# Optimization experiments

Hardware: AMD Instinct MI355X
Metric: run time of the kernel (lower is better)

## Reference

```python
import jax, jax.numpy as jnp
import numpy as np

S_DIM = 512
H2 = 512          # 2 * h_dim, listener feature dim
ATTN = 128
NUM_CLASS = 64
B, T, N = 64, 512, 128
IN_DIM = NUM_CLASS + H2  # LSTM layer-0 input dim


def _p(key, shape, scale=0.05):
    return scale * jax.random.normal(key, shape, dtype=jnp.float32)


def setup_inputs() -> dict:
    key = jax.random.key(0)
    ks = jax.random.split(key, 20)
    inp = {
        "x": jax.random.randint(ks[0], (B, N), 0, NUM_CLASS),
        "h": jax.random.normal(ks[1], (B, T, H2), dtype=jnp.float32),
        # LSTM layer 0 (PyTorch gate order i,f,g,o stacked along dim 0)
        "Wih0": _p(ks[2], (4 * S_DIM, IN_DIM)),
        "Whh0": _p(ks[3], (4 * S_DIM, S_DIM)),
        "bih0": _p(ks[4], (4 * S_DIM,)),
        "bhh0": _p(ks[5], (4 * S_DIM,)),
        # LSTM layer 1
        "Wih1": _p(ks[6], (4 * S_DIM, S_DIM)),
        "Whh1": _p(ks[7], (4 * S_DIM, S_DIM)),
        "bih1": _p(ks[8], (4 * S_DIM,)),
        "bhh1": _p(ks[9], (4 * S_DIM,)),
        # attention projections phi (on s) and psi (on h)
        "Wphi": _p(ks[10], (ATTN, S_DIM)),
        "bphi": _p(ks[11], (ATTN,)),
        "Wpsi": _p(ks[12], (ATTN, H2)),
        "bpsi": _p(ks[13], (ATTN,)),
        # character distribution
        "Wcd": _p(ks[14], (NUM_CLASS, S_DIM + H2)),
        "bcd": _p(ks[15], (NUM_CLASS,)),
    }
    return inp


def _lstm_cell(x, hs, cs, Wih, Whh, bih, bhh):
    g = x @ Wih.T + bih + hs @ Whh.T + bhh
    i, f, gg, o = jnp.split(g, 4, axis=-1)
    c_new = jax.nn.sigmoid(f) * cs + jax.nn.sigmoid(i) * jnp.tanh(gg)
    h_new = jax.nn.sigmoid(o) * jnp.tanh(c_new)
    return h_new, c_new


def reference(x, h, Wih0, Whh0, bih0, bhh0, Wih1, Whh1, bih1, bhh1,
              Wphi, bphi, Wpsi, bpsi, Wcd, bcd):
    # Teacher forcing (tf_rate=1.0): next rnn input char is ground truth x[:, t].
    bs = h.shape[0]
    onehots = jax.nn.one_hot(x, NUM_CLASS, dtype=h.dtype)          # [B, N, C]
    onehots = jnp.transpose(onehots, (1, 0, 2))                    # [N, B, C]
    psi_h = h @ Wpsi.T + bpsi                                      # [B, T, ATTN]

    zeros = jnp.zeros((bs, S_DIM), dtype=h.dtype)
    init = (zeros, zeros, zeros, zeros, h[:, 0, :])                # h1,c1,h2,c2,ctx

    def step(carry, onehot_t):
        h1, c1, h2, c2, ctx = carry
        inp = jnp.concatenate([onehot_t, ctx], axis=-1)            # [B, C+H2]
        h1, c1 = _lstm_cell(inp, h1, c1, Wih0, Whh0, bih0, bhh0)
        h2, c2 = _lstm_cell(h1, h2, c2, Wih1, Whh1, bih1, bhh1)
        s = h2                                                     # [B, S_DIM]
        phi_s = s @ Wphi.T + bphi                                  # [B, ATTN]
        e = jnp.einsum('bd,btd->bt', phi_s, psi_h)                 # [B, T]
        alpha = jax.nn.softmax(e, axis=-1)
        c_ctx = jnp.einsum('bt,btd->bd', alpha, h)                 # [B, H2]
        p = jnp.concatenate([s, c_ctx], axis=-1) @ Wcd.T + bcd     # [B, C]
        return (h1, c1, h2, c2, c_ctx), p

    _, ps = jax.lax.scan(step, init, onehots)                      # [N, B, C]
    return jnp.transpose(ps, (1, 0, 2))                            # [B, N, C]
```

## Files before the change

kernel.cpp:

```cpp
#include <hip/hip_runtime.h>
#include <hip/hip_bf16.h>
#include <math.h>

#define BB 64
#define TT 512
#define NS 128
#define SD 512
#define ATT 128
#define NC 64
#define KX 1024

typedef __attribute__((ext_vector_type(8))) short bf8;
typedef __attribute__((ext_vector_type(4))) float f4;

__device__ __forceinline__ float sigm(float x) { return 1.0f / (1.0f + expf(-x)); }
__device__ __forceinline__ float b2f(short s) {
    union { unsigned u; float f; } c; c.u = ((unsigned)(unsigned short)s) << 16; return c.f;
}
#define MFMA16(a, b, c) __builtin_amdgcn_mfma_f32_16x16x32_bf16((a), (b), (c), 0, 0, 0)

__device__ __forceinline__ void st_sc(__hip_bfloat16* p, float val) {
    __hip_bfloat16 hb(val);
    unsigned short bits; __builtin_memcpy(&bits, &hb, 2);
    unsigned v = bits;
    asm volatile("global_store_short %0, %1, off sc0 sc1" :: "v"(p), "v"(v) : "memory");
}
__device__ __forceinline__ void st_u32_sc(unsigned* p, unsigned v) {
    asm volatile("global_store_dword %0, %1, off sc0 sc1" :: "v"(p), "v"(v) : "memory");
}
__device__ __forceinline__ unsigned ld_u32_sc(const unsigned* p) {
    unsigned v;
    asm volatile("global_load_dword %0, %1, off sc0 sc1\ns_waitcnt vmcnt(0)"
                 : "=v"(v) : "v"(p) : "memory");
    return v;
}

__device__ __forceinline__ void gsync(unsigned* arrv, unsigned* rel, unsigned tk)
{
    __syncthreads();
    if (blockIdx.x == 0) {
        if (threadIdx.x > 0 && threadIdx.x < 256) {
            while (ld_u32_sc(arrv + threadIdx.x * 32) < tk)
                __builtin_amdgcn_s_sleep(2);
        }
        __syncthreads();
        if (threadIdx.x < 8)
            st_u32_sc(rel + threadIdx.x * 32, tk);
    } else {
        if (threadIdx.x == 0) {
            st_u32_sc(arrv + blockIdx.x * 32, tk);
            while (ld_u32_sc(rel + (blockIdx.x & 7) * 32) < tk)
                __builtin_amdgcn_s_sleep(2);
        }
        __syncthreads();
    }
}

template<int BASE>
__device__ __forceinline__ f4 gemm16r(const __hip_bfloat16* Xrow, int quad,
                                      const bf8 (&wreg)[32], f4 acc)
{
    const bf8* Bq = (const bf8*)Xrow + quad;
    bf8 r[16];
#pragma unroll
    for (int i = 0; i < 16; ++i) r[i] = Bq[(BASE + i) * 4];
#pragma unroll
    for (int i = 0; i < 16; ++i) acc = MFMA16(wreg[BASE + i], r[i], acc);
    return acc;
}

__global__ void f2b_kernel(const float* __restrict__ src, __hip_bfloat16* __restrict__ dst, int n)
{
    int i = (blockIdx.x * blockDim.x + threadIdx.x) * 4;
    if (i < n) {
        float4 v = *(const float4*)(src + i);
        dst[i]     = __hip_bfloat16(v.x);
        dst[i + 1] = __hip_bfloat16(v.y);
        dst[i + 2] = __hip_bfloat16(v.z);
        dst[i + 3] = __hip_bfloat16(v.w);
    }
}

__global__ __launch_bounds__(256) void transpose_h_kernel(const float* __restrict__ h,
                                                          __hip_bfloat16* __restrict__ hT)
{
    int bidx = blockIdx.x;
    int b = bidx >> 6, tt0 = ((bidx >> 3) & 7) * 64, dd0 = (bidx & 7) * 64;
    __shared__ __hip_bfloat16 tile[64][65];
    int dd = threadIdx.x & 63, r4 = threadIdx.x >> 6;
#pragma unroll
    for (int i = 0; i < 64; i += 4) {
        int tl = i + r4;
        tile[tl][dd] = __hip_bfloat16(h[((size_t)b * TT + tt0 + tl) * SD + dd0 + dd]);
    }
    __syncthreads();
#pragma unroll
    for (int i = 0; i < 64; i += 4) {
        int dl = i + r4;
        hT[((size_t)b * SD + dd0 + dl) * TT + tt0 + dd] = tile[dd][dl];
    }
}

__global__ void prep_w1_kernel(const float* __restrict__ Wih, const float* __restrict__ Whh,
                               __hip_bfloat16* __restrict__ W)
{
    int idx = blockIdx.x * blockDim.x + threadIdx.x;
    if (idx >= 2048 * KX) return;
    int np = idx >> 10, kk = idx & 1023;
    int q = np & 3, d = np >> 2, j = q * 512 + d;
    float v = (kk < 512) ? Wih[j * 576 + 64 + kk] : Whh[j * 512 + kk - 512];
    W[idx] = __hip_bfloat16(v);
}

__global__ void prep_w2_kernel(const float* __restrict__ Wih, const float* __restrict__ Whh,
                               __hip_bfloat16* __restrict__ W)
{
    int idx = blockIdx.x * blockDim.x + threadIdx.x;
    if (idx >= 2048 * KX) return;
    int np = idx >> 10, kk = idx & 1023;
    int q = np & 3, d = np >> 2, j = q * 512 + d;
    float v = (kk < 512) ? Wih[j * 512 + kk] : Whh[j * 512 + kk - 512];
    W[idx] = __hip_bfloat16(v);
}

__global__ void prep_misc_kernel(const float* __restrict__ Wih0,
                                 const float* __restrict__ bih0, const float* __restrict__ bhh0,
                                 const float* __restrict__ bih1, const float* __restrict__ bhh1,
                                 float* __restrict__ b1v, float* __restrict__ b2v,
                                 float* __restrict__ woh)
{
    int idx = blockIdx.x * blockDim.x + threadIdx.x;
    if (idx >= 64 * 512) return;
    int tok = idx >> 9, d = idx & 511;
    float4 w;
    w.x = Wih0[(0 * 512 + d) * 576 + tok];
    w.y = Wih0[(1 * 512 + d) * 576 + tok];
    w.z = Wih0[(2 * 512 + d) * 576 + tok];
    w.w = Wih0[(3 * 512 + d) * 576 + tok];
    ((float4*)woh)[idx] = w;
    if (tok == 0) {
        float4 b1, b2;
        b1.x = bih0[d] + bhh0[d];             b1.y = bih0[512 + d] + bhh0[512 + d];
        b1.z = bih0[1024 + d] + bhh0[1024 + d]; b1.w = bih0[1536 + d] + bhh0[1536 + d];
        b2.x = bih1[d] + bhh1[d];             b2.y = bih1[512 + d] + bhh1[512 + d];
        b2.z = bih1[1024 + d] + bhh1[1024 + d]; b2.w = bih1[1536 + d] + bhh1[1536 + d];
        ((float4*)b1v)[d] = b1;
        ((float4*)b2v)[d] = b2;
    }
}

__global__ void init_kernel(const float* __restrict__ h,
                            __hip_bfloat16* __restrict__ X1_0,
                            __hip_bfloat16* __restrict__ X2_0,
                            float* __restrict__ c1, float* __restrict__ c2,
                            unsigned* __restrict__ bar)
{
    int idx = blockIdx.x * blockDim.x + threadIdx.x;
    if (idx >= 64 * KX) return;
    int b = idx >> 10, col = idx & 1023;
    __hip_bfloat16 z(0.0f);
    X1_0[idx] = (col < 512) ? __hip_bfloat16(h[(size_t)b * TT * SD + col]) : z;
    X2_0[idx] = z;
    if (idx < 512 * 64) { c1[idx] = 0.f; c2[idx] = 0.f; }
    if (idx < 16384) bar[idx] = 0u;
}

__global__ __launch_bounds__(512, 1) void decode_kernel(
    const __hip_bfloat16* __restrict__ W1, const __hip_bfloat16* __restrict__ W2,
    const __hip_bfloat16* __restrict__ Wphib, const float* __restrict__ bphi,
    const __hip_bfloat16* __restrict__ psib, const __hip_bfloat16* __restrict__ hT,
    __hip_bfloat16* X1base, __hip_bfloat16* X2base,
    __hip_bfloat16* scb, const int* __restrict__ xtok,
    const float* __restrict__ b1v, const float* __restrict__ b2v,
    const float* __restrict__ woh, unsigned* __restrict__ bar)
{
    __shared__ bf8 hTl[128 * 64];
    __shared__ float h2s[512], phis[128], es[512], red[512], wred[16];

    const int bid = blockIdx.x, tid = threadIdx.x;
    const int lane = tid & 63, w = tid >> 6;
    const int mr = lane & 15, quad = lane >> 4;
    const bool isA = bid < 128;
    const int ab = (bid & 7) * 8 + ((bid >> 3) & 7), dch = bid >> 6;

    unsigned* arrv = bar;
    unsigned* rel  = bar + 256 * 32;

    bf8 wreg[32];
    if (tid < 256) {
        const __hip_bfloat16* Wg = isA ? W1 : W2;
        const int m0 = (bid & 127) * 16;
        const bf8* src = (const bf8*)(Wg + (size_t)(m0 + mr) * KX) + quad;
#pragma unroll
        for (int ko = 0; ko < 32; ++ko) wreg[ko] = src[ko * 4];
    }
    {
        const bf8* src = (const bf8*)hT + ((size_t)ab * SD + dch * 128) * 64;
        for (int it = 0; it < 16; ++it) {
            int gidx = it * 512 + tid;
            int d = gidx >> 6, g = gidx & 63;
            hTl[d * 64 + (g ^ (d & 7))] = src[gidx];
        }
    }
    __syncthreads();

    const int dl = (bid & 127) * 4 + quad;
    const int bb = w * 16 + mr;
    const f4 biasv = isA ? ((const f4*)b1v)[dl & 511] : ((const f4*)b2v)[dl & 511];
    const int* xrow = xtok + (bb & 63) * NS;

    float cr = 0.f;
    f4 accP = {0, 0, 0, 0};
    unsigned tk = 0;

    for (int t = 0; t < NS; ++t) {
        __hip_bfloat16* X1c = X1base + (size_t)t * BB * KX;
        __hip_bfloat16* X1n = X1c + (size_t)BB * KX;
        __hip_bfloat16* X2c = X2base + (size_t)t * BB * KX;
        __hip_bfloat16* X2n = X2c + (size_t)BB * KX;

        if (tid < 256) {
            if (isA) {
                f4 wo = ((const f4*)woh)[(size_t)xrow[t] * 512 + dl];
                f4 acc = gemm16r<0>(X1c + (size_t)bb * KX, quad, wreg, accP);
                acc.x += biasv.x + wo.x; acc.y += biasv.y + wo.y;
                acc.z += biasv.z + wo.z; acc.w += biasv.w + wo.w;
                float cn = sigm(acc.y) * cr + sigm(acc.x) * tanhf(acc.z);
                float hn = sigm(acc.w) * tanhf(cn);
                cr = cn;
                st_sc(X2c + (size_t)bb * KX + dl, hn);
                st_sc(X1n + (size_t)bb * KX + 512 + dl, hn);
            } else {
                f4 z = {0, 0, 0, 0};
                accP = gemm16r<16>(X2c + (size_t)bb * KX, quad, wreg, z);
            }
        }
        gsync(arrv, rel, ++tk);

        if (tid < 256) {
            if (isA) {
                f4 z = {0, 0, 0, 0};
                accP = gemm16r<16>(X1n + (size_t)bb * KX, quad, wreg, z);
            } else {
                f4 acc = gemm16r<0>(X2c + (size_t)bb * KX, quad, wreg, accP);
                acc.x += biasv.x; acc.y += biasv.y; acc.z += biasv.z; acc.w += biasv.w;
                float cn = sigm(acc.y) * cr + sigm(acc.x) * tanhf(acc.z);
                float hn = sigm(acc.w) * tanhf(cn);
                cr = cn;
                st_sc(X2n + (size_t)bb * KX + 512 + dl, hn);
                scb[((size_t)bb * NS + t) * 1024 + dl] = __hip_bfloat16(hn);
            }
        }
        gsync(arrv, rel, ++tk);

        {
            if (tid < 64) {
                bf8 v = *((const bf8*)(X2n + (size_t)ab * KX + 512) + tid);
#pragma unroll
                for (int j = 0; j < 8; ++j) h2s[tid * 8 + j] = b2f(v[j]);
            }
            __syncthreads();

            {
                int al = tid & 3, a = tid >> 2;
                const bf8* wr = (const bf8*)(Wphib + (size_t)a * 512) + al;
                float acc = 0.f;
#pragma unroll
                for (int i = 0; i < 16; ++i) {
                    bf8 wv = wr[i * 4];
                    const float* hp2 = h2s + i * 32 + al * 8;
#pragma unroll
                    for (int j = 0; j < 8; ++j) acc += hp2[j] * b2f(wv[j]);
                }
                acc += __shfl_xor(acc, 1);
                acc += __shfl_xor(acc, 2);
                if (al == 0) phis[a] = acc + bphi[a];
            }
            __syncthreads();

            {
                int al = tid & 3;
#pragma unroll
                for (int pass = 0; pass < 4; ++pass) {
                    int tt = pass * 128 + (tid >> 2);
                    const bf8* pr = (const bf8*)(psib + ((size_t)ab * TT + tt) * 128) + al;
                    float acc = 0.f;
#pragma unroll
                    for (int i = 0; i < 4; ++i) {
                        bf8 pv = pr[i * 4];
                        const float* ph = phis + i * 32 + al * 8;
#pragma unroll
                        for (int j = 0; j < 8; ++j) acc += ph[j] * b2f(pv[j]);
                    }
                    acc += __shfl_xor(acc, 1);
                    acc += __shfl_xor(acc, 2);
                    if (al == 0) es[tt] = acc;
                }
            }
            __syncthreads();

            float m = es[tid];
#pragma unroll
            for (int s = 1; s < 64; s <<= 1) m = fmaxf(m, __shfl_xor(m, s));
            if (lane == 0) wred[w] = m;
            __syncthreads();
            float mx = wred[0];
#pragma unroll
            for (int i = 1; i < 8; ++i) mx = fmaxf(mx, wred[i]);
            float e0 = expf(es[tid] - mx);
            es[tid] = e0;
            float s0 = e0;
#pragma unroll
            for (int s = 1; s < 64; s <<= 1) s0 += __shfl_xor(s0, s);
            if (lane == 0) wred[8 + w] = s0;
            __syncthreads();
            float sum = wred[8];
#pragma unroll
            for (int i = 1; i < 8; ++i) sum += wred[8 + i];
            float inv = 1.0f / sum;

            {
                int d = tid & 127, th = tid >> 7;
                const float* ep = es + th * 128;
                const int rb = d * 64, g0 = th * 16, sw = d & 7;
                float a0 = 0.f, a1 = 0.f, a2 = 0.f, a3 = 0.f;
#pragma unroll
                for (int i = 0; i < 16; i += 4) {
                    bf8 v0 = hTl[rb + ((g0 + i)     ^ sw)];
                    bf8 v1 = hTl[rb + ((g0 + i + 1) ^ sw)];
                    bf8 v2 = hTl[rb + ((g0 + i + 2) ^ sw)];
                    bf8 v3 = hTl[rb + ((g0 + i + 3) ^ sw)];
#pragma unroll
                    for (int j = 0; j < 8; ++j) {
                        a0 += ep[i * 8 + j]      * b2f(v0[j]);
                        a1 += ep[i * 8 + 8 + j]  * b2f(v1[j]);
                        a2 += ep[i * 8 + 16 + j] * b2f(v2[j]);
                        a3 += ep[i * 8 + 24 + j] * b2f(v3[j]);
                    }
                }
                red[tid] = (a0 + a1) + (a2 + a3);
                __syncthreads();
                if (th == 0) {
                    float v = (red[d] + red[d + 128] + red[d + 256] + red[d + 384]) * inv;
                    st_sc(X1n + (size_t)ab * KX + dch * 128 + d, v);
                    scb[((size_t)ab * NS + t) * 1024 + 512 + dch * 128 + d] = __hip_bfloat16(v);
                }
            }
        }
        gsync(arrv, rel, ++tk);
    }
}

__global__ __launch_bounds__(256) void fb_lstm0_kernel(
    const __hip_bfloat16* __restrict__ W1, const __hip_bfloat16* __restrict__ X1c,
    __hip_bfloat16* X1n, __hip_bfloat16* X2c, float* __restrict__ c1,
    const float* __restrict__ b1v, const float* __restrict__ woh,
    const int* __restrict__ xtok, int t)
{
    __shared__ __hip_bfloat16 Wlds[32 * 512];
    const int bid = blockIdx.x, tid = threadIdx.x;
    const int lane = tid & 63, w = tid >> 6;
    const int mr = lane & 15, quad = lane >> 4;
    {
        const bf8* src = (const bf8*)(W1 + (size_t)(bid * 16 + mr) * KX) + quad;
        bf8* dstl = (bf8*)Wlds;
        for (int ko = w; ko < 32; ko += 4) dstl[ko * 64 + lane] = src[ko * 4];
    }
    __syncthreads();
    const bf8* Wl = (const bf8*)Wlds + lane;
    const int dl = bid * 4 + quad, bb = w * 16 + mr;
    const bf8* Bq = (const bf8*)(X1c + (size_t)bb * KX) + quad;
    f4 acc = {0, 0, 0, 0};
#pragma unroll
    for (int ko = 0; ko < 32; ++ko) acc = MFMA16(Wl[ko * 64], Bq[ko * 4], acc);
    f4 bv = ((const f4*)b1v)[dl];
    f4 wo = ((const f4*)woh)[(size_t)xtok[bb * NS + t] * 512 + dl];
    acc.x += bv.x + wo.x; acc.y += bv.y + wo.y; acc.z += bv.z + wo.z; acc.w += bv.w + wo.w;
    int ci = dl * 64 + bb;
    float cn = sigm(acc.y) * c1[ci] + sigm(acc.x) * tanhf(acc.z);
    float hn = sigm(acc.w) * tanhf(cn);
    c1[ci] = cn;
    X2c[(size_t)bb * KX + dl] = __hip_bfloat16(hn);
    X1n[(size_t)bb * KX + 512 + dl] = __hip_bfloat16(hn);
}

__global__ __launch_bounds__(256) void fb_lstm1_kernel(
    const __hip_bfloat16* __restrict__ W2, const __hip_bfloat16* __restrict__ X2c,
    __hip_bfloat16* X2n, __hip_bfloat16* scb, float* __restrict__ c2,
    const float* __restrict__ b2v, int t)
{
    __shared__ __hip_bfloat16 Wlds[32 * 512];
    const int bid = blockIdx.x, tid = threadIdx.x;
    const int lane = tid & 63, w = tid >> 6;
    const int mr = lane & 15, quad = lane >> 4;
    {
        const bf8* src = (const bf8*)(W2 + (size_t)(bid * 16 + mr) * KX) + quad;
        bf8* dstl = (bf8*)Wlds;
        for (int ko = w; ko < 32; ko += 4) dstl[ko * 64 + lane] = src[ko * 4];
    }
    __syncthreads();
    const bf8* Wl = (const bf8*)Wlds + lane;
    const int dl = bid * 4 + quad, bb = w * 16 + mr;
    const bf8* Bq = (const bf8*)(X2c + (size_t)bb * KX) + quad;
    f4 acc = {0, 0, 0, 0};
#pragma unroll
    for (int ko = 0; ko < 32; ++ko) acc = MFMA16(Wl[ko * 64], Bq[ko * 4], acc);
    f4 bv = ((const f4*)b2v)[dl];
    acc.x += bv.x; acc.y += bv.y; acc.z += bv.z; acc.w += bv.w;
    int ci = dl * 64 + bb;
    float cn = sigm(acc.y) * c2[ci] + sigm(acc.x) * tanhf(acc.z);
    float hn = sigm(acc.w) * tanhf(cn);
    c2[ci] = cn;
    X2n[(size_t)bb * KX + 512 + dl] = __hip_bfloat16(hn);
    scb[((size_t)bb * NS + t) * 1024 + dl] = __hip_bfloat16(hn);
}

__global__ __launch_bounds__(256) void fb_attn_kernel(
    const __hip_bfloat16* __restrict__ X2n, const __hip_bfloat16* __restrict__ Wphib,
    const float* __restrict__ bphi, const __hip_bfloat16* __restrict__ psib,
    const __hip_bfloat16* __restrict__ hT,
    __hip_bfloat16* X1n, __hip_bfloat16* scb, int t)
{
    __shared__ float h2s[512], phis[128], es[512], red[256];
    int b = blockIdx.x >> 2, dch = blockIdx.x & 3;
    int tid = threadIdx.x;
    if (tid < 64) {
        bf8 v = *((const bf8*)(X2n + (size_t)b * KX + 512) + tid);
#pragma unroll
        for (int j = 0; j < 8; ++j) h2s[tid * 8 + j] = b2f(v[j]);
    }
    __syncthreads();
    {
        int al = tid & 3;
#pragma unroll
        for (int pass = 0; pass < 2; ++pass) {
            int a = pass * 64 + (tid >> 2);
            const bf8* wr = (const bf8*)(Wphib + (size_t)a * 512) + al;
            float acc = 0.f;
#pragma unroll
            for (int i = 0; i < 16; ++i) {
                bf8 wv = wr[i * 4];
                const float* hp2 = h2s + i * 32 + al * 8;
#pragma unroll
                for (int j = 0; j < 8; ++j) acc += hp2[j] * b2f(wv[j]);
            }
            acc += __shfl_xor(acc, 1);
            acc += __shfl_xor(acc, 2);
            if (al == 0) phis[a] = acc + bphi[a];
        }
    }
    __syncthreads();
    {
        int al = tid & 3;
#pragma unroll
        for (int pass = 0; pass < 8; ++pass) {
            int tt = pass * 64 + (tid >> 2);
            const bf8* pr = (const bf8*)(psib + ((size_t)b * TT + tt) * 128) + al;
            float acc = 0.f;
#pragma unroll
            for (int i = 0; i < 4; ++i) {
                bf8 pv = pr[i * 4];
                const float* ph = phis + i * 32 + al * 8;
#pragma unroll
                for (int j = 0; j < 8; ++j) acc += ph[j] * b2f(pv[j]);
            }
            acc += __shfl_xor(acc, 1);
            acc += __shfl_xor(acc, 2);
            if (al == 0) es[tt] = acc;
        }
    }
    __syncthreads();
    red[tid] = fmaxf(es[tid], es[tid + 256]);
    __syncthreads();
    for (int st = 128; st > 0; st >>= 1) {
        if (tid < st) red[tid] = fmaxf(red[tid], red[tid + st]);
        __syncthreads();
    }
    float mx = red[0];
    __syncthreads();
    float e0 = expf(es[tid] - mx), e1 = expf(es[tid + 256] - mx);
    es[tid] = e0; es[tid + 256] = e1;
    red[tid] = e0 + e1;
    __syncthreads();
    for (int st = 128; st > 0; st >>= 1) {
        if (tid < st) red[tid] += red[tid + st];
        __syncthreads();
    }
    float inv = 1.0f / red[0];
    __syncthreads();
    {
        int d = dch * 128 + (tid & 127), th = tid >> 7;
        const bf8* hp = (const bf8*)hT + ((size_t)b * SD + d) * 64 + th * 32;
        const float* ep = es + th * 256;
        float a0 = 0.f, a1 = 0.f, a2 = 0.f, a3 = 0.f;
#pragma unroll
        for (int i = 0; i < 32; i += 4) {
            bf8 v0 = hp[i], v1 = hp[i + 1], v2 = hp[i + 2], v3 = hp[i + 3];
#pragma unroll
            for (int j = 0; j < 8; ++j) {
                a0 += ep[i * 8 + j]      * b2f(v0[j]);
                a1 += ep[i * 8 + 8 + j]  * b2f(v1[j]);
                a2 += ep[i * 8 + 16 + j] * b2f(v2[j]);
                a3 += ep[i * 8 + 24 + j] * b2f(v3[j]);
            }
        }
        float acc = (a0 + a1) + (a2 + a3);
        red[tid] = acc;
        __syncthreads();
        if (th == 0) {
            float v = (acc + red[tid + 128]) * inv;
            X1n[(size_t)b * KX + d] = __hip_bfloat16(v);
            scb[((size_t)b * NS + t) * 1024 + 512 + d] = __hip_bfloat16(v);
        }
    }
}

__global__ __launch_bounds__(256) void psi_gemm_kernel(
    const __hip_bfloat16* __restrict__ A,
    const __hip_bfloat16* __restrict__ Bw,
    const float* __restrict__ bias,
    __hip_bfloat16* __restrict__ C)
{
    int lane = threadIdx.x & 63, wave = threadIdx.x >> 6;
    int m0 = (blockIdx.x * 4 + wave) * 16;
    int mr = lane & 15, quad = lane >> 4;
    const bf8* Ar = (const bf8*)(A + (size_t)(m0 + mr) * 512 + quad * 8);
    f4 acc[8] = {};
    for (int k0 = 0; k0 < 512; k0 += 32) {
        int ko = k0 >> 3;
        bf8 a = Ar[ko];
#pragma unroll
        for (int nf = 0; nf < 8; ++nf) {
            const bf8* Br = (const bf8*)(Bw + (size_t)(nf * 16 + mr) * 512 + quad * 8);
            acc[nf] = MFMA16(a, Br[ko], acc[nf]);
        }
    }
#pragma unroll
    for (int nf = 0; nf < 8; ++nf) {
        int n = nf * 16 + mr;
        float bs = bias[n];
#pragma unroll
        for (int r = 0; r < 4; ++r) {
            int m = m0 + quad * 4 + r;
            C[(size_t)m * 128 + n] = __hip_bfloat16(acc[nf][r] + bs);
        }
    }
}

__global__ __launch_bounds__(256) void out_gemm_kernel(
    const __hip_bfloat16* __restrict__ A,
    const __hip_bfloat16* __restrict__ Bw,
    const float* __restrict__ bias,
    float* __restrict__ C)
{
    int lane = threadIdx.x & 63, wave = threadIdx.x >> 6;
    int m0 = (blockIdx.x * 4 + wave) * 16;
    int mr = lane & 15, quad = lane >> 4;
    const bf8* Ar = (const bf8*)(A + (size_t)(m0 + mr) * 1024 + quad * 8);
    f4 acc[4] = {};
    for (int k0 = 0; k0 < 1024; k0 += 32) {
        int ko = k0 >> 3;
        bf8 a = Ar[ko];
#pragma unroll
        for (int nf = 0; nf < 4; ++nf) {
            const bf8* Br = (const bf8*)(Bw + (size_t)(nf * 16 + mr) * 1024 + quad * 8);
            acc[nf] = MFMA16(a, Br[ko], acc[nf]);
        }
    }
#pragma unroll
    for (int nf = 0; nf < 4; ++nf) {
        int n = nf * 16 + mr;
        float bs = bias[n];
#pragma unroll
        for (int r = 0; r < 4; ++r) {
            int m = m0 + quad * 4 + r;
            C[(size_t)m * 64 + n] = acc[nf][r] + bs;
        }
    }
}

extern "C" void kernel_launch(void* const* d_in, const int* in_sizes, int n_in,
                              void* d_out, int out_size, void* d_ws, size_t ws_size,
                              hipStream_t stream)
{
    const int*   x    = (const int*)  d_in[0];
    const float* h    = (const float*)d_in[1];
    const float* Wih0 = (const float*)d_in[2];
    const float* Whh0 = (const float*)d_in[3];
    const float* bih0 = (const float*)d_in[4];
    const float* bhh0 = (const float*)d_in[5];
    const float* bih1 = (const float*)d_in[8];
    const float* Wih1 = (const float*)d_in[6];
    const float* Whh1 = (const float*)d_in[7];
    const float* bhh1 = (const float*)d_in[9];
    const float* Wphi = (const float*)d_in[10];
    const float* bphi = (const float*)d_in[11];
    const float* Wpsi = (const float*)d_in[12];
    const float* bpsi = (const float*)d_in[13];
    const float* Wcd  = (const float*)d_in[14];
    const float* bcd  = (const float*)d_in[15];
    float* out = (float*)d_out;

    char* p = (char*)d_ws;
    __hip_bfloat16* hbf    = (__hip_bfloat16*)p; p += (size_t)BB * TT * SD * 2;
    __hip_bfloat16* psibf  = (__hip_bfloat16*)p; p += (size_t)BB * TT * ATT * 2;
    __hip_bfloat16* scbf   = (__hip_bfloat16*)p; p += (size_t)BB * NS * 1024 * 2;
    __hip_bfloat16* W1aug  = (__hip_bfloat16*)p; p += (size_t)2048 * KX * 2;
    __hip_bfloat16* W2aug  = (__hip_bfloat16*)p; p += (size_t)2048 * KX * 2;
    __hip_bfloat16* Wphib  = (__hip_bfloat16*)p; p += (size_t)ATT * SD * 2;
    __hip_bfloat16* Wpsib  = (__hip_bfloat16*)p; p += (size_t)ATT * SD * 2;
    __hip_bfloat16* Wcdb   = (__hip_bfloat16*)p; p += (size_t)NC * 1024 * 2;
    __hip_bfloat16* X1base = (__hip_bfloat16*)p; p += (size_t)(NS + 1) * BB * KX * 2;
    __hip_bfloat16* X2base = (__hip_bfloat16*)p; p += (size_t)(NS + 1) * BB * KX * 2;
    float* b1v = (float*)p; p += 512 * 4 * 4;
    float* b2v = (float*)p; p += 512 * 4 * 4;
    float* woh = (float*)p; p += (size_t)64 * 512 * 4 * 4;
    float* c1  = (float*)p; p += (size_t)SD * BB * 4;
    float* c2  = (float*)p; p += (size_t)SD * BB * 4;
    unsigned* bar = (unsigned*)p; p += 16384 * 4;

    f2b_kernel<<<16384, 256, 0, stream>>>(h, hbf, BB * TT * SD);
    f2b_kernel<<<64, 256, 0, stream>>>(Wphi, Wphib, ATT * SD);
    f2b_kernel<<<64, 256, 0, stream>>>(Wpsi, Wpsib, ATT * SD);
    f2b_kernel<<<64, 256, 0, stream>>>(Wcd, Wcdb, NC * 1024);
    prep_w1_kernel<<<(2048 * KX + 255) / 256, 256, 0, stream>>>(Wih0, Whh0, W1aug);
    prep_w2_kernel<<<(2048 * KX + 255) / 256, 256, 0, stream>>>(Wih1, Whh1, W2aug);
    prep_misc_kernel<<<(64 * 512 + 255) / 256, 256, 0, stream>>>(Wih0, bih0, bhh0, bih1, bhh1,
                                                                 b1v, b2v, woh);
    init_kernel<<<(64 * KX + 255) / 256, 256, 0, stream>>>(h, X1base, X2base, c1, c2, bar);
    psi_gemm_kernel<<<512, 256, 0, stream>>>(hbf, Wpsib, bpsi, psibf);
    transpose_h_kernel<<<4096, 256, 0, stream>>>(h, hbf);
    __hip_bfloat16* hT = hbf;

    const __hip_bfloat16 *a0 = W1aug, *a1 = W2aug, *a2 = Wphib;
    const float* a3 = bphi;
    const __hip_bfloat16 *a4 = psibf, *a5 = hT;
    __hip_bfloat16 *a6 = X1base, *a7 = X2base, *a8 = scbf;
    const int* a9 = x;
    const float *a10 = b1v, *a11 = b2v, *a12 = woh;
    unsigned* a13 = bar;
    void* args[14] = {&a0, &a1, &a2, &a3, &a4, &a5, &a6, &a7,
                      &a8, &a9, &a10, &a11, &a12, &a13};
    hipError_t ce = hipLaunchCooperativeKernel((const void*)decode_kernel,
                                               dim3(256), dim3(512), args, 0, stream);
    if (ce != hipSuccess) {
        (void)hipGetLastError();
        for (int t = 0; t < NS; ++t) {
            __hip_bfloat16* X1c = X1base + (size_t)t * BB * KX;
            __hip_bfloat16* X1n = X1c + (size_t)BB * KX;
            __hip_bfloat16* X2c = X2base + (size_t)t * BB * KX;
            __hip_bfloat16* X2n = X2c + (size_t)BB * KX;
            fb_lstm0_kernel<<<128, 256, 0, stream>>>(W1aug, X1c, X1n, X2c, c1, b1v, woh, x, t);
            fb_lstm1_kernel<<<128, 256, 0, stream>>>(W2aug, X2c, X2n, scbf, c2, b2v, t);
            fb_attn_kernel<<<256, 256, 0, stream>>>(X2n, Wphib, bphi, psibf, hT, X1n, scbf, t);
        }
    }
    out_gemm_kernel<<<128, 256, 0, stream>>>(scbf, Wcdb, bcd, out);
}
```

Before: 2.694 ms.

## Replace centralized grid barrier with per-stage producer/consumer flag waits

Replaces the centralized arrive/release grid barrier, which made every block wait on a master block twice per phase, with per-block progress flags for three stages: layer-0 LSTM, layer-1 LSTM and attention. Each consumer polls only the flags of the producers it depends on. This lets B blocks compute the recurrent half of their GEMM before waiting and lets non-critical stores (scb writes) happen after posting. The aim is to cut barrier latency and the serialization through block 0, at the cost of relying on correct flag ordering and memory visibility, which a missed dependency would turn into a race.

```diff
diff --git a/kernel.cpp b/kernel.cpp
--- a/kernel.cpp
+++ b/kernel.cpp
@@ -35,25 +35,19 @@
     return v;
 }
 
-__device__ __forceinline__ void gsync(unsigned* arrv, unsigned* rel, unsigned tk)
-{
-    __syncthreads();
-    if (blockIdx.x == 0) {
-        if (threadIdx.x > 0 && threadIdx.x < 256) {
-            while (ld_u32_sc(arrv + threadIdx.x * 32) < tk)
-                __builtin_amdgcn_s_sleep(2);
-        }
-        __syncthreads();
-        if (threadIdx.x < 8)
-            st_u32_sc(rel + threadIdx.x * 32, tk);
-    } else {
-        if (threadIdx.x == 0) {
-            st_u32_sc(arrv + blockIdx.x * 32, tk);
-            while (ld_u32_sc(rel + (blockIdx.x & 7) * 32) < tk)
-                __builtin_amdgcn_s_sleep(2);
-        }
-        __syncthreads();
-    }
+__device__ __forceinline__ void post_flag(unsigned* flag, unsigned tk)
+{
+    asm volatile("s_waitcnt vmcnt(0)" ::: "memory");
+    __syncthreads();
+    if (threadIdx.x == 0) st_u32_sc(flag, tk);
+}
+__device__ __forceinline__ void wait_flags(const unsigned* f, int n, unsigned tk)
+{
+    if ((int)threadIdx.x < n) {
+        while (ld_u32_sc(f + threadIdx.x * 32) < tk)
+            __builtin_amdgcn_s_sleep(1);
+    }
+    __syncthreads();
 }
 
 template<int BASE>
@@ -183,8 +177,9 @@
     const bool isA = bid < 128;
     const int ab = (bid & 7) * 8 + ((bid >> 3) & 7), dch = bid >> 6;
 
-    unsigned* arrv = bar;
-    unsigned* rel  = bar + 256 * 32;
+    unsigned* fA = bar;
+    unsigned* fB = bar + 128 * 32;
+    unsigned* fC = bar + 256 * 32;
 
     bf8 wreg[32];
     if (tid < 256) {
@@ -211,7 +206,6 @@
 
     float cr = 0.f;
     f4 accP = {0, 0, 0, 0};
-    unsigned tk = 0;
 
     for (int t = 0; t < NS; ++t) {
         __hip_bfloat16* X1c = X1base + (size_t)t * BB * KX;
@@ -219,9 +213,11 @@
         __hip_bfloat16* X2c = X2base + (size_t)t * BB * KX;
         __hip_bfloat16* X2n = X2c + (size_t)BB * KX;
 
-        if (tid < 256) {
-            if (isA) {
-                f4 wo = ((const f4*)woh)[(size_t)xrow[t] * 512 + dl];
+        if (isA) {
+            f4 wo = {0, 0, 0, 0};
+            if (tid < 256) wo = ((const f4*)woh)[(size_t)xrow[t] * 512 + dl];
+            wait_flags(fC, 256, (unsigned)t);
+            if (tid < 256) {
                 f4 acc = gemm16r<0>(X1c + (size_t)bb * KX, quad, wreg, accP);
                 acc.x += biasv.x + wo.x; acc.y += biasv.y + wo.y;
                 acc.z += biasv.z + wo.z; acc.w += biasv.w + wo.w;
@@ -230,29 +226,35 @@
                 cr = cn;
                 st_sc(X2c + (size_t)bb * KX + dl, hn);
                 st_sc(X1n + (size_t)bb * KX + 512 + dl, hn);
-            } else {
-                f4 z = {0, 0, 0, 0};
-                accP = gemm16r<16>(X2c + (size_t)bb * KX, quad, wreg, z);
-            }
-        }
-        gsync(arrv, rel, ++tk);
-
-        if (tid < 256) {
-            if (isA) {
+            }
+            post_flag(fA + bid * 32, (unsigned)(t + 1));
+            wait_flags(fA, 128, (unsigned)(t + 1));
+            if (tid < 256) {
                 f4 z = {0, 0, 0, 0};
                 accP = gemm16r<16>(X1n + (size_t)bb * KX, quad, wreg, z);
-            } else {
-                f4 acc = gemm16r<0>(X2c + (size_t)bb * KX, quad, wreg, accP);
+            }
+        } else {
+            f4 pre = {0, 0, 0, 0};
+            if (tid < 256) {
+                f4 z = {0, 0, 0, 0};
+                pre = gemm16r<16>(X2c + (size_t)bb * KX, quad, wreg, z);
+            }
+            wait_flags(fA, 128, (unsigned)(t + 1));
+            float hnv = 0.f;
+            if (tid < 256) {
+                f4 acc = gemm16r<0>(X2c + (size_t)bb * KX, quad, wreg, pre);
                 acc.x += biasv.x; acc.y += biasv.y; acc.z += biasv.z; acc.w += biasv.w;
                 float cn = sigm(acc.y) * cr + sigm(acc.x) * tanhf(acc.z);
-                float hn = sigm(acc.w) * tanhf(cn);
+                hnv = sigm(acc.w) * tanhf(cn);
                 cr = cn;
-                st_sc(X2n + (size_t)bb * KX + 512 + dl, hn);
-                scb[((size_t)bb * NS + t) * 1024 + dl] = __hip_bfloat16(hn);
-            }
-        }
-        gsync(arrv, rel, ++tk);
-
+                st_sc(X2n + (size_t)bb * KX + 512 + dl, hnv);
+            }
+            post_flag(fB + (bid & 127) * 32, (unsigned)(t + 1));
+            if (tid < 256)
+                scb[((size_t)bb * NS + t) * 1024 + dl] = __hip_bfloat16(hnv);
+        }
+
+        wait_flags(fB, 128, (unsigned)(t + 1));
         {
             if (tid < 64) {
                 bf8 v = *((const bf8*)(X2n + (size_t)ab * KX + 512) + tid);
@@ -340,14 +342,16 @@
                 }
                 red[tid] = (a0 + a1) + (a2 + a3);
                 __syncthreads();
+                float v = 0.f;
                 if (th == 0) {
-                    float v = (red[d] + red[d + 128] + red[d + 256] + red[d + 384]) * inv;
+                    v = (red[d] + red[d + 128] + red[d + 256] + red[d + 384]) * inv;
                     st_sc(X1n + (size_t)ab * KX + dch * 128 + d, v);
+                }
+                post_flag(fC + bid * 32, (unsigned)(t + 1));
+                if (th == 0)
                     scb[((size_t)ab * NS + t) * 1024 + 512 + dch * 128 + d] = __hip_bfloat16(v);
-                }
-            }
-        }
-        gsync(arrv, rel, ++tk);
+            }
+        }
     }
 }
 
@@ -589,9 +593,9 @@
     const float* Whh0 = (const float*)d_in[3];
     const float* bih0 = (const float*)d_in[4];
     const float* bhh0 = (const float*)d_in[5];
-    const float* bih1 = (const float*)d_in[8];
     const float* Wih1 = (const float*)d_in[6];
     const float* Whh1 = (const float*)d_in[7];
+    const float* bih1 = (const float*)d_in[8];
     const float* bhh1 = (const float*)d_in[9];
     const float* Wphi = (const float*)d_in[10];
     const float* bphi = (const float*)d_in[11];
```

Measured after the change: 2.639 ms. -2.0%, faster.
